# Kernel optimization log

Measured on AMD Instinct MI355X. Metric: run time of the kernel, lower is better.

Reference implementation:

```python
import jax, jax.numpy as jnp
import numpy as np

HIDDEN = 2560
NUM_HEADS = 8
NUM_KV_HEADS = 1
HEAD_DIM = 512  # is_full=True -> HEAD_DIM_FULL
MAX_HD = 512
SCALE = 1.0 / float(HEAD_DIM) ** 0.5
SEQ = 32768
SLIDE = 512
CUR_POS = 4000
RING_POS = 100


def setup_inputs() -> dict:
    key = jax.random.key(0)
    ks = jax.random.split(key, 7)
    x = jax.random.normal(ks[0], (1, HIDDEN, 1, 1), jnp.float32)
    kv_full = jax.random.normal(ks[1], (2, NUM_KV_HEADS, SEQ, MAX_HD), jnp.float32) * 0.02
    kv_sliding = jax.random.normal(ks[2], (2, NUM_KV_HEADS, SLIDE, MAX_HD), jnp.float32) * 0.02
    wq = jax.random.normal(ks[3], (NUM_HEADS * HEAD_DIM, HIDDEN), jnp.float32) * 0.02
    wk = jax.random.normal(ks[4], (NUM_KV_HEADS * HEAD_DIM, HIDDEN), jnp.float32) * 0.02
    wv = jax.random.normal(ks[5], (NUM_KV_HEADS * HEAD_DIM, HIDDEN), jnp.float32) * 0.02
    wo = jax.random.normal(ks[6], (HIDDEN, NUM_HEADS * HEAD_DIM), jnp.float32) * 0.02
    return {"x": x, "kv_sliding": kv_sliding, "kv_full": kv_full,
            "wq": wq, "wk": wk, "wv": wv, "wo": wo,
            "current_pos": CUR_POS, "ring_pos": RING_POS}


def reference(x, kv_sliding, kv_full, wq, wk, wv, wo, current_pos, ring_pos):
    # 1x1 convs on a [1,C,1,1] input are plain matvecs
    xv = x.reshape(HIDDEN)
    q = (wq @ xv).reshape(NUM_HEADS, HEAD_DIM)            # [H, D]
    k = (wk @ xv).reshape(NUM_KV_HEADS, HEAD_DIM)         # [1, D]
    v = (wv @ xv).reshape(NUM_KV_HEADS, HEAD_DIM)         # [1, D]
    # is_full=True, slot_idx=0: slice-update write into kv_full at current_pos
    kv_full = jax.lax.dynamic_update_slice(
        kv_full, k[None, :, None, :].astype(kv_full.dtype), (0, 0, current_pos, 0))
    kv_full = jax.lax.dynamic_update_slice(
        kv_full, v[None, :, None, :].astype(kv_full.dtype), (1, 0, current_pos, 0))
    k_cache = kv_full[0, 0, :, :HEAD_DIM]                 # [S, D]
    v_cache = kv_full[1, 0, :, :HEAD_DIM]                 # [S, D]
    # GQA with 1 kv head: repeat == broadcast across the H query heads
    scores = jnp.einsum('hd,sd->hs', q.astype(jnp.float32),
                        k_cache.astype(jnp.float32)) * SCALE   # [H, S]
    probs = jax.nn.softmax(scores, axis=-1)
    attn = jnp.einsum('hs,sd->hd', probs,
                      v_cache.astype(jnp.float32)).astype(x.dtype)  # [H, D]
    out = (wo @ attn.reshape(NUM_HEADS * HEAD_DIM)).reshape(1, HIDDEN, 1, 1)
    return out
```

## Files before the change

kernel.cpp:

```cpp
#include <hip/hip_runtime.h>
#include <stdint.h>

#define HIDDEN 2560
#define NHEADS 8
#define HD 512
#define QDIM (NHEADS * HD)
#define SEQ 32768
#define CHUNK 64
#define NCHUNK (SEQ / CHUNK)
#define PART_ST (8 + NHEADS * HD)
#define SCALE 0.044194173824159216f

#define WS_QKV 0
#define WS_K   4096
#define WS_V   4608
#define WS_ATT 8192
#define WS_PART 16384

__global__ __launch_bounds__(256) void qkv_gemv(
    const float* __restrict__ x,
    const float* __restrict__ wq,
    const float* __restrict__ wk,
    const float* __restrict__ wv,
    float* __restrict__ qkv) {
  const int row = blockIdx.x * 4 + (threadIdx.x >> 6);
  const int lane = threadIdx.x & 63;
  const float* w;
  if (row < QDIM) w = wq + (size_t)row * HIDDEN;
  else if (row < QDIM + HD) w = wk + (size_t)(row - QDIM) * HIDDEN;
  else w = wv + (size_t)(row - QDIM - HD) * HIDDEN;
  float acc = 0.f;
#pragma unroll
  for (int i = 0; i < 5; i++) {
    const int j = i * 512 + lane * 8;
    float4 a0 = *(const float4*)(w + j);
    float4 a1 = *(const float4*)(w + j + 4);
    float4 b0 = *(const float4*)(x + j);
    float4 b1 = *(const float4*)(x + j + 4);
    acc += a0.x * b0.x + a0.y * b0.y + a0.z * b0.z + a0.w * b0.w +
           a1.x * b1.x + a1.y * b1.y + a1.z * b1.z + a1.w * b1.w;
  }
#pragma unroll
  for (int off = 32; off > 0; off >>= 1) acc += __shfl_xor(acc, off);
  if (lane == 0) qkv[row] = acc;
}

__global__ __launch_bounds__(256) void attn_partial(
    const float* __restrict__ kvfull,
    const float* __restrict__ ws,
    const int* __restrict__ cur_pos,
    float* __restrict__ part) {
  __shared__ float sc[CHUNK][NHEADS];
  __shared__ float4 vtmp[NHEADS][128];
  const int tid = threadIdx.x;
  const int lane = tid & 63;
  const int wid = tid >> 6;
  const int cur = cur_pos[0];
  const int s0 = blockIdx.x * CHUNK;
  const float* K = kvfull;
  const float* V = kvfull + (size_t)SEQ * HD;

  float qf[NHEADS][8];
#pragma unroll
  for (int h = 0; h < NHEADS; h++) {
    float4 a = *(const float4*)(ws + WS_QKV + h * HD + lane * 8);
    float4 b = *(const float4*)(ws + WS_QKV + h * HD + lane * 8 + 4);
    qf[h][0] = a.x; qf[h][1] = a.y; qf[h][2] = a.z; qf[h][3] = a.w;
    qf[h][4] = b.x; qf[h][5] = b.y; qf[h][6] = b.z; qf[h][7] = b.w;
  }

  for (int ii = 0; ii < CHUNK / 4; ii++) {
    const int scix = wid * (CHUNK / 4) + ii;
    const int s = s0 + scix;
    const float* krow = (s == cur) ? (ws + WS_K) : (K + (size_t)s * HD);
    float4 a = *(const float4*)(krow + lane * 8);
    float4 b = *(const float4*)(krow + lane * 8 + 4);
    float kb[8] = {a.x, a.y, a.z, a.w, b.x, b.y, b.z, b.w};
    float p[NHEADS];
#pragma unroll
    for (int h = 0; h < NHEADS; h++) {
      float t = 0.f;
#pragma unroll
      for (int e = 0; e < 8; e++) t += kb[e] * qf[h][e];
      p[h] = t;
    }
#pragma unroll
    for (int off = 32; off > 0; off >>= 1) {
#pragma unroll
      for (int h = 0; h < NHEADS; h++) p[h] += __shfl_xor(p[h], off);
    }
    if (lane == 0) {
#pragma unroll
      for (int h = 0; h < NHEADS; h++) sc[scix][h] = __expf(p[h] * SCALE);
    }
  }
  __syncthreads();

  float* pb = part + (size_t)blockIdx.x * PART_ST;
  if (tid < NHEADS) {
    float lsum = 0.f;
    for (int s = 0; s < CHUNK; s++) lsum += sc[s][tid];
    pb[tid] = lsum;
  }

  const int g = tid >> 7;
  const int tl = tid & 127;
  const int d0 = tl * 4;
  float4 acc[NHEADS];
#pragma unroll
  for (int h = 0; h < NHEADS; h++) acc[h] = make_float4(0.f, 0.f, 0.f, 0.f);
  for (int sy = g * (CHUNK / 2); sy < (g + 1) * (CHUNK / 2); sy++) {
    const int s = s0 + sy;
    const float* vrow = (s == cur) ? (ws + WS_V) : (V + (size_t)s * HD);
    float4 v4 = *(const float4*)(vrow + d0);
#pragma unroll
    for (int h = 0; h < NHEADS; h++) {
      const float pp = sc[sy][h];
      acc[h].x += pp * v4.x; acc[h].y += pp * v4.y;
      acc[h].z += pp * v4.z; acc[h].w += pp * v4.w;
    }
  }
  if (g == 1) {
#pragma unroll
    for (int h = 0; h < NHEADS; h++) vtmp[h][tl] = acc[h];
  }
  __syncthreads();
  if (g == 0) {
#pragma unroll
    for (int h = 0; h < NHEADS; h++) {
      float4 o = vtmp[h][tl];
      o.x += acc[h].x; o.y += acc[h].y; o.z += acc[h].z; o.w += acc[h].w;
      *(float4*)(pb + 8 + h * HD + d0) = o;
    }
  }
}

__global__ __launch_bounds__(256) void attn_reduce(
    const float* __restrict__ part,
    float* __restrict__ attn) {
  const int h = blockIdx.x >> 4;
  const int dgrp = blockIdx.x & 15;
  const int tid = threadIdx.x;
  __shared__ float red[256];
  __shared__ float pacc[8][32];

  red[tid] = part[(size_t)tid * PART_ST + h] + part[(size_t)(tid + 256) * PART_ST + h];
  __syncthreads();
  for (int off = 128; off > 0; off >>= 1) {
    if (tid < off) red[tid] += red[tid + off];
    __syncthreads();
  }
  const float Linv = 1.f / red[0];

  const int dloc = tid & 31;
  const int bs = tid >> 5;
  const int d = dgrp * 32 + dloc;
  float acc = 0.f;
#pragma unroll 8
  for (int b = bs * (NCHUNK / 8); b < (bs + 1) * (NCHUNK / 8); b++) {
    acc += part[(size_t)b * PART_ST + 8 + h * HD + d];
  }
  pacc[bs][dloc] = acc;
  __syncthreads();
  if (tid < 32) {
    float s = ((pacc[0][tid] + pacc[1][tid]) + (pacc[2][tid] + pacc[3][tid])) +
              ((pacc[4][tid] + pacc[5][tid]) + (pacc[6][tid] + pacc[7][tid]));
    attn[h * HD + dgrp * 32 + tid] = s * Linv;
  }
}

__global__ __launch_bounds__(256) void out_gemv(
    const float* __restrict__ wo,
    const float* __restrict__ attn,
    float* __restrict__ out) {
  const int row = blockIdx.x * 4 + (threadIdx.x >> 6);
  const int lane = threadIdx.x & 63;
  const float* w = wo + (size_t)row * QDIM;
  float acc = 0.f;
#pragma unroll
  for (int i = 0; i < 8; i++) {
    const int j = i * 512 + lane * 8;
    float4 w0 = *(const float4*)(w + j);
    float4 w1 = *(const float4*)(w + j + 4);
    float4 a0 = *(const float4*)(attn + j);
    float4 a1 = *(const float4*)(attn + j + 4);
    acc += w0.x * a0.x + w0.y * a0.y + w0.z * a0.z + w0.w * a0.w +
           w1.x * a1.x + w1.y * a1.y + w1.z * a1.z + w1.w * a1.w;
  }
#pragma unroll
  for (int off = 32; off > 0; off >>= 1) acc += __shfl_xor(acc, off);
  if (lane == 0) out[row] = acc;
}

extern "C" void kernel_launch(void* const* d_in, const int* in_sizes, int n_in,
                              void* d_out, int out_size, void* d_ws, size_t ws_size,
                              hipStream_t stream) {
  (void)in_sizes; (void)n_in; (void)out_size; (void)ws_size;
  const float* x      = (const float*)d_in[0];
  const float* kvfull = (const float*)d_in[2];
  const float* wq     = (const float*)d_in[3];
  const float* wk     = (const float*)d_in[4];
  const float* wv     = (const float*)d_in[5];
  const float* wo     = (const float*)d_in[6];
  const int* cur_pos  = (const int*)d_in[7];
  float* out = (float*)d_out;
  float* ws = (float*)d_ws;

  qkv_gemv<<<(QDIM + 2 * HD) / 4, 256, 0, stream>>>(x, wq, wk, wv, ws + WS_QKV);
  attn_partial<<<NCHUNK, 256, 0, stream>>>(kvfull, ws, cur_pos, ws + WS_PART);
  attn_reduce<<<NHEADS * 16, 256, 0, stream>>>(ws + WS_PART, ws + WS_ATT);
  out_gemv<<<HIDDEN / 4, 256, 0, stream>>>(wo, ws + WS_ATT, out);
}
```

Baseline: 281.7 us.

## Fuse score and value passes per wave with register accumulation in attention partial

Each wave now owns 16 sequence rows and, in a single loop, loads the K and V rows together. It computes the 8 head scores, exponentiates them, and accumulates the denominators and weighted V directly in registers. The block then reduces the four per-wave partials through a 64 KB shared buffer, replacing the score staging array and the separate V pass. The aim is to cut the second pass, the intermediate barrier and redundant LDS score reads, and to keep more memory loads in flight. In exchange, register pressure and LDS use per block rise, which may lower occupancy.

Result: no change. 280.4 us (-0.4%).

```diff
diff --git a/kernel.cpp b/kernel.cpp
--- a/kernel.cpp
+++ b/kernel.cpp
@@ -50,13 +50,13 @@
     const float* __restrict__ ws,
     const int* __restrict__ cur_pos,
     float* __restrict__ part) {
-  __shared__ float sc[CHUNK][NHEADS];
-  __shared__ float4 vtmp[NHEADS][128];
+  __shared__ float accbuf[4][NHEADS * HD];
+  __shared__ float denbuf[4][NHEADS];
   const int tid = threadIdx.x;
   const int lane = tid & 63;
   const int wid = tid >> 6;
   const int cur = cur_pos[0];
-  const int s0 = blockIdx.x * CHUNK;
+  const int s0 = blockIdx.x * CHUNK + wid * 16;
   const float* K = kvfull;
   const float* V = kvfull + (size_t)SEQ * HD;
 
@@ -69,13 +69,25 @@
     qf[h][4] = b.x; qf[h][5] = b.y; qf[h][6] = b.z; qf[h][7] = b.w;
   }
 
-  for (int ii = 0; ii < CHUNK / 4; ii++) {
-    const int scix = wid * (CHUNK / 4) + ii;
-    const int s = s0 + scix;
-    const float* krow = (s == cur) ? (ws + WS_K) : (K + (size_t)s * HD);
-    float4 a = *(const float4*)(krow + lane * 8);
-    float4 b = *(const float4*)(krow + lane * 8 + 4);
-    float kb[8] = {a.x, a.y, a.z, a.w, b.x, b.y, b.z, b.w};
+  float acc[NHEADS][8];
+#pragma unroll
+  for (int h = 0; h < NHEADS; h++)
+#pragma unroll
+    for (int e = 0; e < 8; e++) acc[h][e] = 0.f;
+  float den[NHEADS];
+#pragma unroll
+  for (int h = 0; h < NHEADS; h++) den[h] = 0.f;
+
+#pragma unroll 2
+  for (int u = 0; u < 16; u++) {
+    const int s = s0 + u;
+    const float* kr = (s == cur) ? (ws + WS_K) : (K + (size_t)s * HD);
+    const float* vr = (s == cur) ? (ws + WS_V) : (V + (size_t)s * HD);
+    float4 k0 = *(const float4*)(kr + lane * 8);
+    float4 k1 = *(const float4*)(kr + lane * 8 + 4);
+    float4 v0 = *(const float4*)(vr + lane * 8);
+    float4 v1 = *(const float4*)(vr + lane * 8 + 4);
+    const float kb[8] = {k0.x, k0.y, k0.z, k0.w, k1.x, k1.y, k1.z, k1.w};
     float p[NHEADS];
 #pragma unroll
     for (int h = 0; h < NHEADS; h++) {
@@ -89,49 +101,41 @@
 #pragma unroll
       for (int h = 0; h < NHEADS; h++) p[h] += __shfl_xor(p[h], off);
     }
-    if (lane == 0) {
-#pragma unroll
-      for (int h = 0; h < NHEADS; h++) sc[scix][h] = __expf(p[h] * SCALE);
+#pragma unroll
+    for (int h = 0; h < NHEADS; h++) {
+      const float pe = __expf(p[h] * SCALE);
+      den[h] += pe;
+      acc[h][0] += pe * v0.x; acc[h][1] += pe * v0.y;
+      acc[h][2] += pe * v0.z; acc[h][3] += pe * v0.w;
+      acc[h][4] += pe * v1.x; acc[h][5] += pe * v1.y;
+      acc[h][6] += pe * v1.z; acc[h][7] += pe * v1.w;
     }
   }
+
+#pragma unroll
+  for (int h = 0; h < NHEADS; h++) {
+    float4 lo = make_float4(acc[h][0], acc[h][1], acc[h][2], acc[h][3]);
+    float4 hi = make_float4(acc[h][4], acc[h][5], acc[h][6], acc[h][7]);
+    *(float4*)(&accbuf[wid][h * HD + lane * 8])     = lo;
+    *(float4*)(&accbuf[wid][h * HD + lane * 8 + 4]) = hi;
+  }
+  if (lane == 0) {
+#pragma unroll
+    for (int h = 0; h < NHEADS; h++) denbuf[wid][h] = den[h];
+  }
   __syncthreads();
 
   float* pb = part + (size_t)blockIdx.x * PART_ST;
-  if (tid < NHEADS) {
-    float lsum = 0.f;
-    for (int s = 0; s < CHUNK; s++) lsum += sc[s][tid];
-    pb[tid] = lsum;
-  }
-
-  const int g = tid >> 7;
-  const int tl = tid & 127;
-  const int d0 = tl * 4;
-  float4 acc[NHEADS];
-#pragma unroll
-  for (int h = 0; h < NHEADS; h++) acc[h] = make_float4(0.f, 0.f, 0.f, 0.f);
-  for (int sy = g * (CHUNK / 2); sy < (g + 1) * (CHUNK / 2); sy++) {
-    const int s = s0 + sy;
-    const float* vrow = (s == cur) ? (ws + WS_V) : (V + (size_t)s * HD);
-    float4 v4 = *(const float4*)(vrow + d0);
-#pragma unroll
-    for (int h = 0; h < NHEADS; h++) {
-      const float pp = sc[sy][h];
-      acc[h].x += pp * v4.x; acc[h].y += pp * v4.y;
-      acc[h].z += pp * v4.z; acc[h].w += pp * v4.w;
-    }
-  }
-  if (g == 1) {
-#pragma unroll
-    for (int h = 0; h < NHEADS; h++) vtmp[h][tl] = acc[h];
-  }
-  __syncthreads();
-  if (g == 0) {
-#pragma unroll
-    for (int h = 0; h < NHEADS; h++) {
-      float4 o = vtmp[h][tl];
-      o.x += acc[h].x; o.y += acc[h].y; o.z += acc[h].z; o.w += acc[h].w;
-      *(float4*)(pb + 8 + h * HD + d0) = o;
-    }
+  if (tid < NHEADS)
+    pb[tid] = denbuf[0][tid] + denbuf[1][tid] + denbuf[2][tid] + denbuf[3][tid];
+  for (int i = tid; i < QDIM / 4; i += 256) {
+    float4 a = *(float4*)(&accbuf[0][i * 4]);
+    float4 b = *(float4*)(&accbuf[1][i * 4]);
+    float4 c = *(float4*)(&accbuf[2][i * 4]);
+    float4 d = *(float4*)(&accbuf[3][i * 4]);
+    a.x += b.x + c.x + d.x; a.y += b.y + c.y + d.y;
+    a.z += b.z + c.z + d.z; a.w += b.w + c.w + d.w;
+    *(float4*)(pb + 8 + i * 4) = a;
   }
 }
 
```
